# Optimization experiments

Measured on AMD Instinct MI355X. Metric: run time of the kernel, lower is better.

Reference implementation:

```python
import jax, jax.numpy as jnp
import numpy as np

B, S, D, H = 2, 2048, 1024, 16
DK = D // H


def setup_inputs() -> dict:
    key = jax.random.key(0)
    ks = jax.random.split(key, 11)
    s = 1.0 / np.sqrt(D)
    return {
        "q": jax.random.normal(ks[0], (B, S, D), jnp.float32),
        "k": jax.random.normal(ks[1], (B, S, D), jnp.float32),
        "v": jax.random.normal(ks[2], (B, S, D), jnp.float32),
        "mask": jnp.ones((B, 1, S, S), jnp.int32),
        "Wq": jax.random.normal(ks[3], (D, D), jnp.float32) * s,
        "bq": jnp.zeros((D,), jnp.float32),
        "Wk": jax.random.normal(ks[4], (D, D), jnp.float32) * s,
        "bk": jnp.zeros((D,), jnp.float32),
        "Wv": jax.random.normal(ks[5], (D, D), jnp.float32) * s,
        "bv": jnp.zeros((D,), jnp.float32),
        "Wo": jax.random.normal(ks[6], (D, D), jnp.float32) * s,
        "bo": jnp.zeros((D,), jnp.float32),
    }


def reference(q, k, v, mask, Wq, bq, Wk, bk, Wv, bv, Wo, bo):
    # Note: original torch code calls non-in-place masked_fill and discards the
    # result, so the mask has no mathematical effect; we preserve that.
    qh = (q @ Wq + bq).reshape(B, S, H, DK).transpose(0, 2, 1, 3)  # [B,H,S,DK]
    kh = (k @ Wk + bk).reshape(B, S, H, DK).transpose(0, 2, 1, 3)
    vh = (v @ Wv + bv).reshape(B, S, H, DK).transpose(0, 2, 1, 3)
    scores = jnp.einsum("bhqd,bhkd->bhqk", qh, kh) / jnp.sqrt(jnp.float32(DK))
    attn = jax.nn.softmax(scores, axis=-1)
    out = jnp.einsum("bhqk,bhkd->bhqd", attn, vh)  # [B,H,S,DK]
    out = out.transpose(0, 2, 1, 3).reshape(B, S, D)
    return out @ Wo + bo
```

## Files before the change

kernel.cpp:

```cpp
#include <hip/hip_runtime.h>

#define S_LEN    2048
#define D_MODEL  1024
#define N_HEADS  16
#define HEAD_DIM 64
#define BATCH    2

typedef __bf16 bf16x8 __attribute__((ext_vector_type(8)));
typedef float  floatx4 __attribute__((ext_vector_type(4)));

__device__ __forceinline__ unsigned short f2bf(float f) {
    union { float f; unsigned int u; } v;
    v.f = f;
    unsigned int u = v.u;
    u += 0x7fffu + ((u >> 16) & 1u);
    return (unsigned short)(u >> 16);
}

__device__ __forceinline__ unsigned int pk_rne(float a, float b) {
    union { float f; unsigned int u; } ua, ub;
    ua.f = a; ub.f = b;
    unsigned int x = ua.u + 0x7fffu + ((ua.u >> 16) & 1u);
    unsigned int y = ub.u + 0x7fffu + ((ub.u >> 16) & 1u);
    return __builtin_amdgcn_perm(y, x, 0x07060302);
}

__device__ __forceinline__ void gload_lds16(const unsigned short* g, unsigned short* l) {
    __builtin_amdgcn_global_load_lds(
        (const __attribute__((address_space(1))) void*)(const void*)g,
        (__attribute__((address_space(3))) void*)(void*)l,
        16, 0, 0);
}

struct PrepArgs {
    const float* W[4];   unsigned short* Wt[4];
};

__global__ void prep_kernel(PrepArgs args) {
    __shared__ unsigned short tile[64][65];
    const int r  = blockIdx.x;
    const int w  = r >> 8;
    const int xy = r & 255;
    const int n0 = (xy & 15) * 64, k0 = (xy >> 4) * 64;
    const float* W = args.W[w];
    unsigned short* Wt = args.Wt[w];
    for (int rep = 0; rep < 16; ++rep) {
        int e = rep * 256 + threadIdx.x;
        int kk = e >> 6, nn = e & 63;
        tile[kk][nn] = f2bf(W[(size_t)(k0 + kk) * D_MODEL + n0 + nn]);
    }
    __syncthreads();
    for (int rep = 0; rep < 16; ++rep) {
        int e = rep * 256 + threadIdx.x;
        int nn = e >> 6, kk = e & 63;
        Wt[(size_t)(n0 + nn) * D_MODEL + k0 + kk] = tile[kk][nn];
    }
}

template <int TM, int TN, int MODE, bool AF32>
__device__ __forceinline__
void gemm_body(const void* __restrict__ A,
               const unsigned short* __restrict__ Bt,
               const float* __restrict__ bias,
               void* __restrict__ out,
               int m0, int n0, float scale,
               unsigned short* As, unsigned short* Bs) {
    constexpr int MT = TM / 32;
    constexpr int NT = TN / 32;
    const int tid  = threadIdx.x;
    const int wid  = tid >> 6;
    const int lane = tid & 63;

    floatx4 acc[MT][NT];
#pragma unroll
    for (int i = 0; i < MT; ++i)
#pragma unroll
        for (int j = 0; j < NT; ++j) acc[i][j] = (floatx4)0.0f;

    const int srow = lane >> 3;
    const int gch  = (lane & 7) ^ srow;
    const int wr = (wid >> 1) * (TM / 2);
    const int wc = (wid & 1) * (TN / 2);
    const int fr = lane & 15;
    const int fq = lane >> 4;
    const int sw7 = fr & 7;

    for (int k0 = 0; k0 < D_MODEL; k0 += 64) {
        if (k0) __syncthreads();

        float4 fa[MT > 0 ? TM / 32 : 1][2];
        if constexpr (AF32) {
#pragma unroll
            for (int ci = 0; ci < TM / 32; ++ci) {
                const int c = wid + ci * 4;
                const float* src = (const float*)A + (size_t)(m0 + c * 8 + srow) * D_MODEL + k0 + gch * 8;
                fa[ci][0] = reinterpret_cast<const float4*>(src)[0];
                fa[ci][1] = reinterpret_cast<const float4*>(src)[1];
            }
        }
#pragma unroll
        for (int ci = TM / 32; ci < (TM + TN) / 32; ++ci) {
            const int cb = wid + ci * 4 - TM / 8;
            const int row = cb * 8 + srow;
            gload_lds16(Bt + (size_t)(n0 + row) * D_MODEL + k0 + gch * 8, Bs + cb * 512);
        }
        if constexpr (AF32) {
#pragma unroll
            for (int ci = 0; ci < TM / 32; ++ci) {
                const int c = wid + ci * 4;
                uint4 wv;
                wv.x = pk_rne(fa[ci][0].x, fa[ci][0].y); wv.y = pk_rne(fa[ci][0].z, fa[ci][0].w);
                wv.z = pk_rne(fa[ci][1].x, fa[ci][1].y); wv.w = pk_rne(fa[ci][1].z, fa[ci][1].w);
                *reinterpret_cast<uint4*>(As + c * 512 + lane * 8) = wv;
            }
        } else {
#pragma unroll
            for (int ci = 0; ci < TM / 32; ++ci) {
                const int c = wid + ci * 4;
                const int row = c * 8 + srow;
                gload_lds16((const unsigned short*)A + (size_t)(m0 + row) * D_MODEL + k0 + gch * 8,
                            As + c * 512);
            }
        }
        __syncthreads();

#pragma unroll
        for (int kk = 0; kk < 2; ++kk) {
            bf16x8 af[MT], bfv[NT];
#pragma unroll
            for (int t = 0; t < MT; ++t)
                af[t] = *reinterpret_cast<const bf16x8*>(
                    As + (wr + t * 16 + fr) * 64 + (((kk * 4 + fq) ^ sw7) * 8));
#pragma unroll
            for (int t = 0; t < NT; ++t)
                bfv[t] = *reinterpret_cast<const bf16x8*>(
                    Bs + (wc + t * 16 + fr) * 64 + (((kk * 4 + fq) ^ sw7) * 8));
#pragma unroll
            for (int mt = 0; mt < MT; ++mt)
#pragma unroll
                for (int nt = 0; nt < NT; ++nt)
                    acc[mt][nt] = __builtin_amdgcn_mfma_f32_16x16x32_bf16(af[mt], bfv[nt], acc[mt][nt], 0, 0, 0);
        }
    }

#pragma unroll
    for (int nt = 0; nt < NT; ++nt) {
        const int n = n0 + wc + nt * 16 + fr;
        const float bval = bias[n];
#pragma unroll
        for (int mt = 0; mt < MT; ++mt) {
#pragma unroll
            for (int r = 0; r < 4; ++r) {
                const int m = m0 + wr + mt * 16 + fq * 4 + r;
                const float val = (acc[mt][nt][r] + bval) * scale;
                if (MODE == 2) {
                    reinterpret_cast<float*>(out)[(size_t)m * D_MODEL + n] = val;
                } else {
                    const int b = m >> 11, s = m & (S_LEN - 1);
                    const int h = n >> 6, dk = n & 63;
                    const unsigned short o16 = f2bf(val);
                    if (MODE == 0)
                        reinterpret_cast<unsigned short*>(out)[(((size_t)(b * N_HEADS + h)) * S_LEN + s) * HEAD_DIM + dk] = o16;
                    else
                        reinterpret_cast<unsigned short*>(out)[(((size_t)(b * N_HEADS + h)) * HEAD_DIM + dk) * S_LEN + s] = o16;
                }
            }
        }
    }
}

struct QKVArgs {
    const float* A[3];
    const unsigned short* Bt[3];
    const float* bias[3];
    unsigned short* out[3];
};

__global__ __launch_bounds__(256)
void qkv_gemm_kernel(QKVArgs args) {
    __shared__ __align__(16) unsigned short As[128 * 64];
    __shared__ __align__(16) unsigned short Bs[128 * 64];
    const int z  = blockIdx.z;
    const int wg = blockIdx.x + (blockIdx.y << 3);
    const int t  = ((wg & 7) << 5) + (wg >> 3);
    const int n0 = (t & 7) * 128;
    const int m0 = (t >> 3) * 128;
    if (z == 0)
        gemm_body<128, 128, 0, true>(args.A[0], args.Bt[0], args.bias[0], args.out[0], m0, n0, 0.18033688011112f, As, Bs);
    else if (z == 1)
        gemm_body<128, 128, 0, true>(args.A[1], args.Bt[1], args.bias[1], args.out[1], m0, n0, 1.0f, As, Bs);
    else
        gemm_body<128, 128, 1, true>(args.A[2], args.Bt[2], args.bias[2], args.out[2], m0, n0, 1.0f, As, Bs);
}

__global__ __launch_bounds__(256)
void oproj_gemm_kernel(const unsigned short* __restrict__ A,
                       const unsigned short* __restrict__ Bt,
                       const float* __restrict__ bias,
                       float* __restrict__ out) {
    __shared__ __align__(16) unsigned short As[64 * 64];
    __shared__ __align__(16) unsigned short Bs[128 * 64];
    const int wg = blockIdx.x + (blockIdx.y << 3);
    const int t  = ((wg & 7) << 6) + (wg >> 3);
    const int n0 = (t & 7) * 128;
    const int m0 = (t >> 3) * 64;
    gemm_body<64, 128, 2, false>(A, Bt, bias, out, m0, n0, 1.0f, As, Bs);
}

__global__ __launch_bounds__(128)
void attn_kernel(const unsigned short* __restrict__ qhp,
                 const unsigned short* __restrict__ khp,
                 const unsigned short* __restrict__ vtp,
                 unsigned short* __restrict__ outp) {
    __shared__ __align__(16) unsigned short Qs[64 * 64];
    __shared__ __align__(16) unsigned short Ks[64 * 64];
    __shared__ __align__(16) unsigned short Vs[64 * 64];
    __shared__ __align__(16) unsigned short Ps[2][32 * 72];

    const int tid  = threadIdx.x;
    const int wid  = tid >> 6;
    const int lane = tid & 63;
    const int b = blockIdx.z, h = blockIdx.y;
    const int q0 = blockIdx.x * 64;

    const unsigned short* qbase = qhp + (size_t)(b * N_HEADS + h) * S_LEN * HEAD_DIM;
    const unsigned short* kbase = khp + (size_t)(b * N_HEADS + h) * S_LEN * HEAD_DIM;
    const unsigned short* vbase = vtp + (size_t)(b * N_HEADS + h) * HEAD_DIM * S_LEN;

    const int srow = lane >> 3;
    const int gch  = (lane & 7) ^ srow;
    const int fr = lane & 15;
    const int fq = lane >> 4;
    const int sw7 = fr & 7;

#pragma unroll
    for (int i = 0; i < 4; ++i) {
        const int c = wid * 4 + i;
        const int row = c * 8 + srow;
        gload_lds16(qbase + (size_t)(q0 + row) * HEAD_DIM + gch * 8, Qs + c * 512);
    }
    __syncthreads();

    bf16x8 qf[2][2];
#pragma unroll
    for (int qh2 = 0; qh2 < 2; ++qh2)
#pragma unroll
        for (int kk = 0; kk < 2; ++kk)
            qf[qh2][kk] = *reinterpret_cast<const bf16x8*>(
                Qs + (wid * 32 + qh2 * 16 + fr) * 64 + (((kk * 4 + fq) ^ sw7) * 8));

    floatx4 o_acc[2][4];
#pragma unroll
    for (int i = 0; i < 2; ++i)
#pragma unroll
        for (int j = 0; j < 4; ++j) o_acc[i][j] = (floatx4)0.0f;
    float l_sum[2] = {0.0f, 0.0f};

    for (int kv0 = 0; kv0 < S_LEN; kv0 += 64) {
        if (kv0) __syncthreads();
#pragma unroll
        for (int i = 0; i < 4; ++i) {
            const int c = wid * 4 + i;
            const int row = c * 8 + srow;
            gload_lds16(kbase + (size_t)(kv0 + row) * HEAD_DIM + gch * 8, Ks + c * 512);
            gload_lds16(vbase + (size_t)row * S_LEN + kv0 + gch * 8,       Vs + c * 512);
        }
        __syncthreads();

        floatx4 st[2][4];
#pragma unroll
        for (int i = 0; i < 2; ++i)
#pragma unroll
            for (int j = 0; j < 4; ++j) st[i][j] = (floatx4)0.0f;
#pragma unroll
        for (int nt = 0; nt < 4; ++nt) {
#pragma unroll
            for (int kk = 0; kk < 2; ++kk) {
                bf16x8 kf = *reinterpret_cast<const bf16x8*>(
                    Ks + (nt * 16 + fr) * 64 + (((kk * 4 + fq) ^ sw7) * 8));
                st[0][nt] = __builtin_amdgcn_mfma_f32_16x16x32_bf16(kf, qf[0][kk], st[0][nt], 0, 0, 0);
                st[1][nt] = __builtin_amdgcn_mfma_f32_16x16x32_bf16(kf, qf[1][kk], st[1][nt], 0, 0, 0);
            }
        }

#pragma unroll
        for (int qh2 = 0; qh2 < 2; ++qh2) {
#pragma unroll
            for (int nt = 0; nt < 4; ++nt) {
                float p0 = __builtin_amdgcn_exp2f(st[qh2][nt][0]);
                float p1 = __builtin_amdgcn_exp2f(st[qh2][nt][1]);
                float p2 = __builtin_amdgcn_exp2f(st[qh2][nt][2]);
                float p3 = __builtin_amdgcn_exp2f(st[qh2][nt][3]);
                l_sum[qh2] += (p0 + p1) + (p2 + p3);
                uint2 w;
                w.x = pk_rne(p0, p1);
                w.y = pk_rne(p2, p3);
                *reinterpret_cast<uint2*>(Ps[wid] + (qh2 * 16 + fr) * 72 + nt * 16 + fq * 4) = w;
            }
        }
        __asm__ volatile("s_waitcnt lgkmcnt(0)" ::: "memory");

#pragma unroll
        for (int kk = 0; kk < 2; ++kk) {
            bf16x8 pf0 = *reinterpret_cast<const bf16x8*>(Ps[wid] + (fr)      * 72 + kk * 32 + fq * 8);
            bf16x8 pf1 = *reinterpret_cast<const bf16x8*>(Ps[wid] + (16 + fr) * 72 + kk * 32 + fq * 8);
#pragma unroll
            for (int dt = 0; dt < 4; ++dt) {
                bf16x8 vf = *reinterpret_cast<const bf16x8*>(
                    Vs + (dt * 16 + fr) * 64 + (((kk * 4 + fq) ^ sw7) * 8));
                o_acc[0][dt] = __builtin_amdgcn_mfma_f32_16x16x32_bf16(pf0, vf, o_acc[0][dt], 0, 0, 0);
                o_acc[1][dt] = __builtin_amdgcn_mfma_f32_16x16x32_bf16(pf1, vf, o_acc[1][dt], 0, 0, 0);
            }
        }
    }

#pragma unroll
    for (int qh2 = 0; qh2 < 2; ++qh2) {
        float l = l_sum[qh2];
        l += __shfl_xor(l, 16);
        l += __shfl_xor(l, 32);
        float linv[4];
#pragma unroll
        for (int r = 0; r < 4; ++r)
            linv[r] = __builtin_amdgcn_rcpf(__shfl(l, fq * 4 + r));
#pragma unroll
        for (int dt = 0; dt < 4; ++dt) {
#pragma unroll
            for (int r = 0; r < 4; ++r) {
                const int s  = q0 + wid * 32 + qh2 * 16 + fq * 4 + r;
                const int dk = dt * 16 + fr;
                const float val = o_acc[qh2][dt][r] * linv[r];
                outp[((size_t)(b * S_LEN + s)) * D_MODEL + h * HEAD_DIM + dk] = f2bf(val);
            }
        }
    }
}

extern "C" void kernel_launch(void* const* d_in, const int* in_sizes, int n_in,
                              void* d_out, int out_size, void* d_ws, size_t ws_size,
                              hipStream_t stream) {
    (void)in_sizes; (void)n_in; (void)out_size; (void)ws_size;
    const float* q  = (const float*)d_in[0];
    const float* k  = (const float*)d_in[1];
    const float* v  = (const float*)d_in[2];
    const float* Wq = (const float*)d_in[4];
    const float* bq = (const float*)d_in[5];
    const float* Wk = (const float*)d_in[6];
    const float* bk = (const float*)d_in[7];
    const float* Wv = (const float*)d_in[8];
    const float* bv = (const float*)d_in[9];
    const float* Wo = (const float*)d_in[10];
    const float* bo = (const float*)d_in[11];
    float* out = (float*)d_out;

    char* ws = (char*)d_ws;
    const size_t SZ_ACT = (size_t)BATCH * S_LEN * D_MODEL * 2;
    const size_t SZ_W   = (size_t)D_MODEL * D_MODEL * 2;
    unsigned short* attn = (unsigned short*)(ws);
    unsigned short* Wqt  = (unsigned short*)(ws + 3 * SZ_ACT);
    unsigned short* Wkt  = (unsigned short*)(ws + 3 * SZ_ACT + SZ_W);
    unsigned short* Wvt  = (unsigned short*)(ws + 3 * SZ_ACT + 2 * SZ_W);
    unsigned short* Wot  = (unsigned short*)(ws + 3 * SZ_ACT + 3 * SZ_W);
    unsigned short* qhb  = (unsigned short*)(ws + 3 * SZ_ACT + 4 * SZ_W);
    unsigned short* khb  = (unsigned short*)(ws + 4 * SZ_ACT + 4 * SZ_W);
    unsigned short* vtb  = (unsigned short*)(ws + 5 * SZ_ACT + 4 * SZ_W);

    PrepArgs pargs;
    pargs.W[0] = Wq;  pargs.W[1] = Wk;  pargs.W[2] = Wv;  pargs.W[3] = Wo;
    pargs.Wt[0] = Wqt; pargs.Wt[1] = Wkt; pargs.Wt[2] = Wvt; pargs.Wt[3] = Wot;
    prep_kernel<<<dim3(1024), 256, 0, stream>>>(pargs);

    QKVArgs gargs;
    gargs.A[0] = q;  gargs.A[1] = k;  gargs.A[2] = v;
    gargs.Bt[0] = Wqt; gargs.Bt[1] = Wkt; gargs.Bt[2] = Wvt;
    gargs.bias[0] = bq; gargs.bias[1] = bk; gargs.bias[2] = bv;
    gargs.out[0] = qhb; gargs.out[1] = khb; gargs.out[2] = vtb;
    qkv_gemm_kernel<<<dim3(8, 32, 3), 256, 0, stream>>>(gargs);

    attn_kernel<<<dim3(S_LEN / 64, N_HEADS, BATCH), 128, 0, stream>>>(qhb, khb, vtb, attn);

    oproj_gemm_kernel<<<dim3(8, 64), 256, 0, stream>>>(attn, Wot, bo, out);
}
```

Baseline: 252.6 us.

## Double-buffer LDS tiles in QKV and output-projection GEMMs

Measured after the change: 284.2 us. 1.13x slower.

```diff
diff --git a/kernel.cpp b/kernel.cpp
--- a/kernel.cpp
+++ b/kernel.cpp
@@ -64,9 +64,12 @@
                const float* __restrict__ bias,
                void* __restrict__ out,
                int m0, int n0, float scale,
-               unsigned short* As, unsigned short* Bs) {
-    constexpr int MT = TM / 32;
-    constexpr int NT = TN / 32;
+               unsigned short* As0, unsigned short* Bs0) {
+    constexpr int MT   = TM / 32;
+    constexpr int NT   = TN / 32;
+    constexpr int ABUF = TM * 64;
+    constexpr int BBUF = TN * 64;
+    constexpr int NIT  = D_MODEL / 64;
     const int tid  = threadIdx.x;
     const int wid  = tid >> 6;
     const int lane = tid & 63;
@@ -85,44 +88,66 @@
     const int fq = lane >> 4;
     const int sw7 = fr & 7;
 
-    for (int k0 = 0; k0 < D_MODEL; k0 += 64) {
-        if (k0) __syncthreads();
-
-        float4 fa[MT > 0 ? TM / 32 : 1][2];
-        if constexpr (AF32) {
-#pragma unroll
-            for (int ci = 0; ci < TM / 32; ++ci) {
-                const int c = wid + ci * 4;
-                const float* src = (const float*)A + (size_t)(m0 + c * 8 + srow) * D_MODEL + k0 + gch * 8;
-                fa[ci][0] = reinterpret_cast<const float4*>(src)[0];
-                fa[ci][1] = reinterpret_cast<const float4*>(src)[1];
-            }
-        }
-#pragma unroll
-        for (int ci = TM / 32; ci < (TM + TN) / 32; ++ci) {
-            const int cb = wid + ci * 4 - TM / 8;
-            const int row = cb * 8 + srow;
-            gload_lds16(Bt + (size_t)(n0 + row) * D_MODEL + k0 + gch * 8, Bs + cb * 512);
-        }
-        if constexpr (AF32) {
-#pragma unroll
-            for (int ci = 0; ci < TM / 32; ++ci) {
-                const int c = wid + ci * 4;
-                uint4 wv;
-                wv.x = pk_rne(fa[ci][0].x, fa[ci][0].y); wv.y = pk_rne(fa[ci][0].z, fa[ci][0].w);
-                wv.z = pk_rne(fa[ci][1].x, fa[ci][1].y); wv.w = pk_rne(fa[ci][1].z, fa[ci][1].w);
-                *reinterpret_cast<uint4*>(As + c * 512 + lane * 8) = wv;
-            }
-        } else {
-#pragma unroll
-            for (int ci = 0; ci < TM / 32; ++ci) {
-                const int c = wid + ci * 4;
-                const int row = c * 8 + srow;
-                gload_lds16((const unsigned short*)A + (size_t)(m0 + row) * D_MODEL + k0 + gch * 8,
-                            As + c * 512);
-            }
-        }
-        __syncthreads();
+    if constexpr (AF32) {
+#pragma unroll
+        for (int ci = 0; ci < MT; ++ci) {
+            const int c = wid + ci * 4;
+            const float* src = (const float*)A + (size_t)(m0 + c * 8 + srow) * D_MODEL + gch * 8;
+            float4 f0 = reinterpret_cast<const float4*>(src)[0];
+            float4 f1 = reinterpret_cast<const float4*>(src)[1];
+            uint4 wv;
+            wv.x = pk_rne(f0.x, f0.y); wv.y = pk_rne(f0.z, f0.w);
+            wv.z = pk_rne(f1.x, f1.y); wv.w = pk_rne(f1.z, f1.w);
+            *reinterpret_cast<uint4*>(As0 + c * 512 + lane * 8) = wv;
+        }
+    } else {
+#pragma unroll
+        for (int ci = 0; ci < MT; ++ci) {
+            const int c = wid + ci * 4;
+            gload_lds16((const unsigned short*)A + (size_t)(m0 + c * 8 + srow) * D_MODEL + gch * 8,
+                        As0 + c * 512);
+        }
+    }
+#pragma unroll
+    for (int ci = 0; ci < NT; ++ci) {
+        const int cb = wid + ci * 4;
+        gload_lds16(Bt + (size_t)(n0 + cb * 8 + srow) * D_MODEL + gch * 8, Bs0 + cb * 512);
+    }
+    __syncthreads();
+
+    for (int it = 0; it < NIT; ++it) {
+        const int cur = it & 1;
+        unsigned short* Ac = As0 + cur * ABUF;
+        unsigned short* Bc = Bs0 + cur * BBUF;
+        unsigned short* An = As0 + (cur ^ 1) * ABUF;
+        unsigned short* Bn = Bs0 + (cur ^ 1) * BBUF;
+        const int kn = (it + 1) * 64;
+        const bool pf = (it + 1 < NIT);
+
+        float4 fa[MT][2];
+        if (pf) {
+            if constexpr (AF32) {
+#pragma unroll
+                for (int ci = 0; ci < MT; ++ci) {
+                    const int c = wid + ci * 4;
+                    const float* src = (const float*)A + (size_t)(m0 + c * 8 + srow) * D_MODEL + kn + gch * 8;
+                    fa[ci][0] = reinterpret_cast<const float4*>(src)[0];
+                    fa[ci][1] = reinterpret_cast<const float4*>(src)[1];
+                }
+            } else {
+#pragma unroll
+                for (int ci = 0; ci < MT; ++ci) {
+                    const int c = wid + ci * 4;
+                    gload_lds16((const unsigned short*)A + (size_t)(m0 + c * 8 + srow) * D_MODEL + kn + gch * 8,
+                                An + c * 512);
+                }
+            }
+#pragma unroll
+            for (int ci = 0; ci < NT; ++ci) {
+                const int cb = wid + ci * 4;
+                gload_lds16(Bt + (size_t)(n0 + cb * 8 + srow) * D_MODEL + kn + gch * 8, Bn + cb * 512);
+            }
+        }
 
 #pragma unroll
         for (int kk = 0; kk < 2; ++kk) {
@@ -130,16 +155,30 @@
 #pragma unroll
             for (int t = 0; t < MT; ++t)
                 af[t] = *reinterpret_cast<const bf16x8*>(
-                    As + (wr + t * 16 + fr) * 64 + (((kk * 4 + fq) ^ sw7) * 8));
+                    Ac + (wr + t * 16 + fr) * 64 + (((kk * 4 + fq) ^ sw7) * 8));
 #pragma unroll
             for (int t = 0; t < NT; ++t)
                 bfv[t] = *reinterpret_cast<const bf16x8*>(
-                    Bs + (wc + t * 16 + fr) * 64 + (((kk * 4 + fq) ^ sw7) * 8));
+                    Bc + (wc + t * 16 + fr) * 64 + (((kk * 4 + fq) ^ sw7) * 8));
 #pragma unroll
             for (int mt = 0; mt < MT; ++mt)
 #pragma unroll
                 for (int nt = 0; nt < NT; ++nt)
                     acc[mt][nt] = __builtin_amdgcn_mfma_f32_16x16x32_bf16(af[mt], bfv[nt], acc[mt][nt], 0, 0, 0);
+        }
+
+        if (pf) {
+            if constexpr (AF32) {
+#pragma unroll
+                for (int ci = 0; ci < MT; ++ci) {
+                    const int c = wid + ci * 4;
+                    uint4 wv;
+                    wv.x = pk_rne(fa[ci][0].x, fa[ci][0].y); wv.y = pk_rne(fa[ci][0].z, fa[ci][0].w);
+                    wv.z = pk_rne(fa[ci][1].x, fa[ci][1].y); wv.w = pk_rne(fa[ci][1].z, fa[ci][1].w);
+                    *reinterpret_cast<uint4*>(An + c * 512 + lane * 8) = wv;
+                }
+            }
+            __syncthreads();
         }
     }
 
@@ -178,19 +217,20 @@
 
 __global__ __launch_bounds__(256)
 void qkv_gemm_kernel(QKVArgs args) {
-    __shared__ __align__(16) unsigned short As[128 * 64];
-    __shared__ __align__(16) unsigned short Bs[128 * 64];
+    __shared__ __align__(16) unsigned short smem[4 * 128 * 64];
+    unsigned short* As0 = smem;
+    unsigned short* Bs0 = smem + 2 * 128 * 64;
     const int z  = blockIdx.z;
     const int wg = blockIdx.x + (blockIdx.y << 3);
     const int t  = ((wg & 7) << 5) + (wg >> 3);
     const int n0 = (t & 7) * 128;
     const int m0 = (t >> 3) * 128;
     if (z == 0)
-        gemm_body<128, 128, 0, true>(args.A[0], args.Bt[0], args.bias[0], args.out[0], m0, n0, 0.18033688011112f, As, Bs);
+        gemm_body<128, 128, 0, true>(args.A[0], args.Bt[0], args.bias[0], args.out[0], m0, n0, 0.18033688011112f, As0, Bs0);
     else if (z == 1)
-        gemm_body<128, 128, 0, true>(args.A[1], args.Bt[1], args.bias[1], args.out[1], m0, n0, 1.0f, As, Bs);
+        gemm_body<128, 128, 0, true>(args.A[1], args.Bt[1], args.bias[1], args.out[1], m0, n0, 1.0f, As0, Bs0);
     else
-        gemm_body<128, 128, 1, true>(args.A[2], args.Bt[2], args.bias[2], args.out[2], m0, n0, 1.0f, As, Bs);
+        gemm_body<128, 128, 1, true>(args.A[2], args.Bt[2], args.bias[2], args.out[2], m0, n0, 1.0f, As0, Bs0);
 }
 
 __global__ __launch_bounds__(256)
@@ -198,13 +238,14 @@
                        const unsigned short* __restrict__ Bt,
                        const float* __restrict__ bias,
                        float* __restrict__ out) {
-    __shared__ __align__(16) unsigned short As[64 * 64];
-    __shared__ __align__(16) unsigned short Bs[128 * 64];
+    __shared__ __align__(16) unsigned short smem[2 * 64 * 64 + 2 * 128 * 64];
+    unsigned short* As0 = smem;
+    unsigned short* Bs0 = smem + 2 * 64 * 64;
     const int wg = blockIdx.x + (blockIdx.y << 3);
     const int t  = ((wg & 7) << 6) + (wg >> 3);
     const int n0 = (t & 7) * 128;
     const int m0 = (t >> 3) * 64;
-    gemm_body<64, 128, 2, false>(A, Bt, bias, out, m0, n0, 1.0f, As, Bs);
+    gemm_body<64, 128, 2, false>(A, Bt, bias, out, m0, n0, 1.0f, As0, Bs0);
 }
 
 __global__ __launch_bounds__(128)
```
